# Kernel tuning notes

Measured on AMD Instinct MI355X. Metric: run time of the kernel, lower is better.

## Reference

```python
import jax, jax.numpy as jnp
import numpy as np

HID, NH, HD = 1024, 16, 64
WIN = 512
DFF, NE, TOPK = 4096, 8, 2
B, S = 1, 2048
EPS = 1e-6


def _rope_rotation_matrix(seq_len, head_dim):
    # Block-diagonal 2x2 rotation matrices per position (standard RoPE as a fused matrix).
    pos = np.arange(seq_len, dtype=np.float64)
    inv_freq = 1.0 / (10000.0 ** (np.arange(0, head_dim, 2, dtype=np.float64) / head_dim))
    ang = pos[:, None] * inv_freq[None, :]            # [S, HD/2]
    c, s = np.cos(ang), np.sin(ang)
    R = np.zeros((seq_len, head_dim, head_dim), np.float32)
    i = np.arange(0, head_dim, 2)
    R[:, i, i] = c
    R[:, i + 1, i + 1] = c
    R[:, i, i + 1] = -s
    R[:, i + 1, i] = s
    return jnp.asarray(R)


def setup_inputs() -> dict:
    key = jax.random.key(0)
    ks = jax.random.split(key, 10)
    init = lambda k, shape, scale=0.02: (jax.random.normal(k, shape, jnp.float32) * scale)
    return {
        "x": jax.random.normal(ks[0], (B, S, HID), jnp.float32),
        "rotation_matrix": _rope_rotation_matrix(S, HD),
        "rms1_w": jnp.ones((HID,), jnp.float32),
        "wq": init(ks[1], (HID, HID)),
        "wk": init(ks[2], (HID, HID)),
        "wv": init(ks[3], (HID, HID)),
        "wo": init(ks[4], (HID, HID)),
        "rms2_w": jnp.ones((HID,), jnp.float32),
        "gate_w": init(ks[5], (HID, NE)),
        "w1": init(ks[6], (NE, HID, DFF)),
        "w2": init(ks[7], (NE, DFF, HID)),
        "w3": init(ks[8], (NE, HID, DFF)),
    }


def _rmsnorm(x, w):
    return x * jax.lax.rsqrt(jnp.mean(x * x, axis=-1, keepdims=True) + EPS) * w


def reference(x, rotation_matrix, rms1_w, wq, wk, wv, wo, rms2_w, gate_w, w1, w2, w3):
    b, s, _ = x.shape
    # --- sliding-window attention with fused RoPE rotation matrix ---
    y = _rmsnorm(x, rms1_w)
    q = (y @ wq).reshape(b, s, NH, HD).transpose(0, 2, 1, 3)  # bhsd
    k = (y @ wk).reshape(b, s, NH, HD).transpose(0, 2, 1, 3)
    v = (y @ wv).reshape(b, s, NH, HD).transpose(0, 2, 1, 3)
    q = jnp.einsum('bhsd,sde->bhse', q, rotation_matrix)
    k = jnp.einsum('bhsd,sde->bhse', k, rotation_matrix)
    scores = jnp.einsum('bhqd,bhkd->bhqk', q, k) / np.float32(np.sqrt(HD))
    idx = jnp.arange(s)
    mask = (idx[:, None] >= idx[None, :]) & (idx[:, None] - idx[None, :] < WIN)
    scores = jnp.where(mask[None, None], scores, jnp.float32(-1e9))
    att = jax.nn.softmax(scores, axis=-1)
    attn_out = jnp.einsum('bhqk,bhkd->bhqd', att, v)
    attn_out = attn_out.transpose(0, 2, 1, 3).reshape(b, s, HID) @ wo
    x = x + attn_out
    # --- MoE SwiGLU FFN with top-k routing ---
    y = _rmsnorm(x, rms2_w)
    t = y.reshape(b * s, HID)                                  # [T, D]
    logits = t @ gate_w                                        # [T, E]
    top_v, top_i = jax.lax.top_k(logits, TOPK)
    gates = jax.nn.softmax(top_v, axis=-1)                     # [T, K]
    w_full = jnp.zeros((b * s, NE), t.dtype).at[
        jnp.arange(b * s)[:, None], top_i].set(gates)          # [T, E] sparse routing weights
    h = jax.nn.silu(jnp.einsum('td,edf->etf', t, w1)) * jnp.einsum('td,edf->etf', t, w3)
    expert_out = jnp.einsum('etf,efd->etd', h, w2)             # [E, T, D]
    moe = jnp.einsum('te,etd->td', w_full, expert_out).reshape(b, s, HID)
    return x + moe
```

## Files before the change

kernel.cpp:

```cpp
#include <hip/hip_runtime.h>
#include <hip/hip_bf16.h>
#include <stdint.h>


#define S_ 2048
#define HID_ 1024
#define NH_ 16
#define HD_ 64
#define WIN_ 512
#define DFF_ 4096
#define NE_ 8

typedef unsigned short u16;
typedef __attribute__((ext_vector_type(8))) short short8;
typedef __attribute__((ext_vector_type(4))) float f32x4;

__device__ __forceinline__ u16 f2bf(float f) {
  union { float f; unsigned u; } v; v.f = f;
  unsigned r = (v.u + 0x7FFFu + ((v.u >> 16) & 1u)) >> 16;
  return (u16)r;
}
__device__ __forceinline__ float bf2f(u16 b) {
  union { unsigned u; float f; } v; v.u = ((unsigned)b) << 16;
  return v.f;
}

__device__ __forceinline__ void gload16(const void* g, void* l) {
  __builtin_amdgcn_global_load_lds(
      (const __attribute__((address_space(1))) void*)g,
      (__attribute__((address_space(3))) void*)l, 16, 0, 0);
}

template <int N>
__device__ __forceinline__ void waitcnt_vm() {
  static_assert(N == 0 || N == 2 || N == 4 || N == 6 || N == 8 || N == 12 ||
                N == 16 || N == 24, "unsupported vmcnt");
  if constexpr (N == 0) asm volatile("s_waitcnt vmcnt(0)" ::: "memory");
  else if constexpr (N == 2) asm volatile("s_waitcnt vmcnt(2)" ::: "memory");
  else if constexpr (N == 4) asm volatile("s_waitcnt vmcnt(4)" ::: "memory");
  else if constexpr (N == 6) asm volatile("s_waitcnt vmcnt(6)" ::: "memory");
  else if constexpr (N == 8) asm volatile("s_waitcnt vmcnt(8)" ::: "memory");
  else if constexpr (N == 12) asm volatile("s_waitcnt vmcnt(12)" ::: "memory");
  else if constexpr (N == 16) asm volatile("s_waitcnt vmcnt(16)" ::: "memory");
  else if constexpr (N == 24) asm volatile("s_waitcnt vmcnt(24)" ::: "memory");
}

__global__ __launch_bounds__(512) void convT_f32_k(const float* __restrict__ Wa,
                                                   const float* __restrict__ Wb,
                                                   int zsplit,
                                                   u16* __restrict__ WT,
                                                   int K, int N, size_t matStride) {
  __shared__ alignas(16) char T[256 * 264];
  int z = blockIdx.z;
  const float* Wm = (z < zsplit ? Wa + (size_t)z * matStride
                                : Wb + (size_t)(z - zsplit) * matStride);
  u16* WTm = WT + (size_t)z * matStride;
  int n0 = blockIdx.x * 128, k0 = blockIdx.y * 256;
  int tid = threadIdx.x;
  int mq = tid & 31, tr_ = tid >> 5;
#pragma unroll
  for (int p = 0; p < 16; ++p) {
    int k = p * 16 + tr_;
    float4 v = *(const float4*)&Wm[(size_t)(k0 + k) * N + n0 + mq * 4];
    uint2 pk;
    pk.x = (unsigned)f2bf(v.x) | ((unsigned)f2bf(v.y) << 16);
    pk.y = (unsigned)f2bf(v.z) | ((unsigned)f2bf(v.w) << 16);
    *(uint2*)(T + k * 264 + ((mq ^ ((k >> 2) & 31)) << 3)) = pk;
  }
  __syncthreads();
#pragma unroll
  for (int p = 0; p < 8; ++p) {
    int n = p * 16 + tr_;
    int un = n >> 2, lo2 = (n & 3) * 2;
    short8 o;
#pragma unroll
    for (int j = 0; j < 8; ++j) {
      int k = mq * 8 + j;
      ((u16*)&o)[j] =
          *(const u16*)(T + k * 264 + ((un ^ ((k >> 2) & 31)) << 3) + lo2);
    }
    *(short8*)&WTm[(size_t)(n0 + n) * K + k0 + mq * 8] = o;
  }
}

__global__ __launch_bounds__(512) void convT_qkvo_k(const float* __restrict__ wq,
                                                    const float* __restrict__ wk,
                                                    const float* __restrict__ wv,
                                                    const float* __restrict__ wo,
                                                    u16* __restrict__ outT) {
  __shared__ alignas(16) char T[256 * 264];
  int z = blockIdx.z;
  const float* Wm = (z == 0) ? wq : (z == 1) ? wk : (z == 2) ? wv : wo;
  u16* WTm = outT + (size_t)z * HID_ * HID_;
  int n0 = blockIdx.x * 128, k0 = blockIdx.y * 256;
  int tid = threadIdx.x;
  int mq = tid & 31, tr_ = tid >> 5;
#pragma unroll
  for (int p = 0; p < 16; ++p) {
    int k = p * 16 + tr_;
    float4 v = *(const float4*)&Wm[(size_t)(k0 + k) * HID_ + n0 + mq * 4];
    uint2 pk;
    pk.x = (unsigned)f2bf(v.x) | ((unsigned)f2bf(v.y) << 16);
    pk.y = (unsigned)f2bf(v.z) | ((unsigned)f2bf(v.w) << 16);
    *(uint2*)(T + k * 264 + ((mq ^ ((k >> 2) & 31)) << 3)) = pk;
  }
  __syncthreads();
#pragma unroll
  for (int p = 0; p < 8; ++p) {
    int n = p * 16 + tr_;
    int un = n >> 2, lo2 = (n & 3) * 2;
    short8 o;
#pragma unroll
    for (int j = 0; j < 8; ++j) {
      int k = mq * 8 + j;
      ((u16*)&o)[j] =
          *(const u16*)(T + k * 264 + ((un ^ ((k >> 2) & 31)) << 3) + lo2);
    }
    *(short8*)&WTm[(size_t)(n0 + n) * HID_ + k0 + mq * 8] = o;
  }
}

__global__ __launch_bounds__(256) void convT_u16_k(const u16* __restrict__ W,
                                                   u16* __restrict__ WT,
                                                   int K, int N, size_t matStride) {
  __shared__ u16 t[64][66];
  const u16* Wm = W + (size_t)blockIdx.z * matStride;
  u16* WTm = WT + (size_t)blockIdx.z * matStride;
  int n0 = blockIdx.x * 64, k0 = blockIdx.y * 64;
  int tid = threadIdx.x;
  int c2 = (tid & 31) * 2, rr = tid >> 5;
#pragma unroll
  for (int it = 0; it < 8; ++it) {
    int r = it * 8 + rr;
    unsigned vv = *(const unsigned*)&Wm[(size_t)(k0 + r) * N + n0 + c2];
    t[c2][r] = (u16)vv;
    t[c2 + 1][r] = (u16)(vv >> 16);
  }
  __syncthreads();
#pragma unroll
  for (int it = 0; it < 8; ++it) {
    int n = it * 8 + rr;
    unsigned pk = (unsigned)t[n][c2] | ((unsigned)t[n][c2 + 1] << 16);
    *(unsigned*)&WTm[(size_t)(n0 + n) * K + k0 + c2] = pk;
  }
}

__global__ __launch_bounds__(256) void rms1_rope_k(const float* __restrict__ x,
                                                   const float* __restrict__ rw,
                                                   u16* __restrict__ y,
                                                   const float* __restrict__ rot,
                                                   float* __restrict__ cost,
                                                   float* __restrict__ sint) {
  int b = blockIdx.x, tid = threadIdx.x;
  if (b >= S_) {
    int id = (b - S_) * 256 + tid;
    if (id < S_ * 32) {
      int s = id >> 5, j = id & 31;
      cost[id] = rot[(size_t)s * 4096 + (size_t)(2 * j) * 64 + 2 * j];
      sint[id] = rot[(size_t)s * 4096 + (size_t)(2 * j + 1) * 64 + 2 * j];
    }
    return;
  }
  int row = b;
  const float4 v = *(const float4*)&x[(size_t)row * HID_ + tid * 4];
  float ss = v.x * v.x + v.y * v.y + v.z * v.z + v.w * v.w;
#pragma unroll
  for (int o = 32; o; o >>= 1) ss += __shfl_xor(ss, o);
  __shared__ float red[4];
  if ((tid & 63) == 0) red[tid >> 6] = ss;
  __syncthreads();
  float rstd = rsqrtf((red[0] + red[1] + red[2] + red[3]) * (1.f / HID_) + 1e-6f);
  const float4 w4 = *(const float4*)&rw[tid * 4];
  ushort4 o4;
  o4.x = f2bf(v.x * rstd * w4.x);
  o4.y = f2bf(v.y * rstd * w4.y);
  o4.z = f2bf(v.z * rstd * w4.z);
  o4.w = f2bf(v.w * rstd * w4.w);
  *(ushort4*)&y[(size_t)row * HID_ + tid * 4] = o4;
}

__global__ __launch_bounds__(256) void rms2_gate_k(const float* __restrict__ x2,
                                                   const float* __restrict__ rw,
                                                   const float* __restrict__ gw,
                                                   u16* __restrict__ y2,
                                                   float* __restrict__ logits) {
  int row = blockIdx.x, tid = threadIdx.x;
  int wv = tid >> 6, ln = tid & 63;
  const float4 v = *(const float4*)&x2[(size_t)row * HID_ + tid * 4];
  float ss = v.x * v.x + v.y * v.y + v.z * v.z + v.w * v.w;
#pragma unroll
  for (int o = 32; o; o >>= 1) ss += __shfl_xor(ss, o);
  __shared__ float red[4];
  __shared__ float lred[4][8];
  if (ln == 0) red[wv] = ss;
  __syncthreads();
  float rstd = rsqrtf((red[0] + red[1] + red[2] + red[3]) * (1.f / HID_) + 1e-6f);
  const float4 w4 = *(const float4*)&rw[tid * 4];
  float yv[4];
  yv[0] = v.x * rstd * w4.x; yv[1] = v.y * rstd * w4.y;
  yv[2] = v.z * rstd * w4.z; yv[3] = v.w * rstd * w4.w;
  ushort4 o4;
  o4.x = f2bf(yv[0]); o4.y = f2bf(yv[1]); o4.z = f2bf(yv[2]); o4.w = f2bf(yv[3]);
  *(ushort4*)&y2[(size_t)row * HID_ + tid * 4] = o4;
  float le[8] = {0, 0, 0, 0, 0, 0, 0, 0};
  int d0 = tid * 4;
#pragma unroll
  for (int j = 0; j < 4; ++j) {
    const float* grow = &gw[(size_t)(d0 + j) * NE_];
#pragma unroll
    for (int e = 0; e < 8; ++e) le[e] += yv[j] * grow[e];
  }
#pragma unroll
  for (int e = 0; e < 8; ++e) {
    float t = le[e];
#pragma unroll
    for (int o = 32; o; o >>= 1) t += __shfl_xor(t, o);
    le[e] = t;
  }
  if (ln == 0)
#pragma unroll
    for (int e = 0; e < 8; ++e) lred[wv][e] = le[e];
  __syncthreads();
  if (tid < 8)
    logits[(size_t)row * NE_ + tid] =
        lred[0][tid] + lred[1][tid] + lred[2][tid] + lred[3][tid];
}

__global__ __launch_bounds__(1024) void route_k(const float* __restrict__ logits,
                                                int* __restrict__ topi,
                                                float* __restrict__ topg,
                                                int* __restrict__ counts,
                                                int* __restrict__ ebase,
                                                int* __restrict__ slot_token,
                                                int* __restrict__ slot_of) {
  __shared__ int cnt[8], bas[8], rnk[8];
  int tid = threadIdx.x;
  if (tid < 8) { cnt[tid] = 0; rnk[tid] = 0; }
  __syncthreads();
  int e0[2], e1[2];
  float g0[2], g1[2];
#pragma unroll
  for (int s = 0; s < 2; ++s) {
    int t = tid * 2 + s;
    const float* lg = &logits[(size_t)t * NE_];
    float v0 = -1e30f; int i0 = 0;
#pragma unroll
    for (int e = 0; e < 8; ++e) {
      float x = lg[e];
      if (x > v0) { v0 = x; i0 = e; }
    }
    float v1 = -1e30f; int i1 = 0;
#pragma unroll
    for (int e = 0; e < 8; ++e) {
      if (e == i0) continue;
      float x = lg[e];
      if (x > v1) { v1 = x; i1 = e; }
    }
    float ex = __expf(v1 - v0);
    e0[s] = i0; e1[s] = i1;
    g0[s] = 1.f / (1.f + ex);
    g1[s] = ex / (1.f + ex);
    topi[t * 2] = i0; topi[t * 2 + 1] = i1;
    topg[t * 2] = g0[s]; topg[t * 2 + 1] = g1[s];
    atomicAdd(&cnt[i0], 1);
    atomicAdd(&cnt[i1], 1);
  }
  __syncthreads();
  if (tid == 0) {
    int s = 0;
    for (int e = 0; e < 8; ++e) { bas[e] = s; s += cnt[e]; }
  }
  __syncthreads();
#pragma unroll
  for (int s = 0; s < 2; ++s) {
    int t = tid * 2 + s;
    int p0 = bas[e0[s]] + atomicAdd(&rnk[e0[s]], 1);
    int p1 = bas[e1[s]] + atomicAdd(&rnk[e1[s]], 1);
    slot_token[p0] = t; slot_token[p1] = t;
    slot_of[t * 2] = p0; slot_of[t * 2 + 1] = p1;
  }
  if (tid < 8) { counts[tid] = cnt[tid]; ebase[tid] = bas[tid]; }
}

template <int MODE, int SLOTS>
__global__ __launch_bounds__(256, (SLOTS <= 3 ? 3 : (SLOTS <= 5 ? 2 : 1)))
void gemm3_k(
    const u16* __restrict__ A, const u16* __restrict__ B0,
    const u16* __restrict__ B1, const u16* __restrict__ B2, int K,
    const int* __restrict__ ecnt, const int* __restrict__ ebase,
    const float* __restrict__ cost, const float* __restrict__ sint,
    const float* __restrict__ xres, float* __restrict__ outf,
    u16* __restrict__ o0, u16* __restrict__ o1, u16* __restrict__ o2) {
  constexpr int WVM = 4 * (SLOTS - 2);
  __shared__ alignas(16) char smem[SLOTS * 16384];

  int n0 = blockIdx.x * 128, m0 = blockIdx.y * 128;
  int cnt = 0, base = 0, kc = 0;
  const u16* Bp;
  u16* outb = o0;
  float* pout = outf;
  int rope = 0;
  if constexpr (MODE == 0) {
    int z = blockIdx.z;
    Bp = (z == 0) ? B0 : (z == 1) ? B1 : B2;
    outb = (z == 0) ? o0 : (z == 1) ? o1 : o2;
    rope = (z < 2) ? 1 : 0;
  } else if constexpr (MODE == 1) {
    Bp = B0;
  } else if constexpr (MODE == 4) {
    int e = blockIdx.z >> 1;
    kc = blockIdx.z & 1;
    cnt = ecnt[e]; base = ebase[e];
    if (m0 >= cnt) return;
    Bp = B0 + (size_t)e * HID_ * DFF_;
    pout = outf + (size_t)kc * ((size_t)2 * S_ * HID_);
  } else {
    int e = blockIdx.z;
    cnt = ecnt[e]; base = ebase[e];
    if (m0 >= cnt) return;
    Bp = B0 + (size_t)e * HID_ * DFF_;
  }

  int tid = threadIdx.x, w = tid >> 6, l = tid & 63, lo = l & 15, g = l >> 4;
  int wm = w >> 1, wn = w & 1;
  int KT = K >> 5;
  size_t rb = (MODE == 4) ? (size_t)DFF_ * 2 : (size_t)K * 2;
  size_t kcoff = (MODE == 4) ? (size_t)kc * (size_t)(DFF_ / 2) * 2 : 0;

  int lrow = l >> 2, lu = l & 3;
  const char* pA[2];
  const char* pB[2];
  int ldOff[2];
#pragma unroll
  for (int j = 0; j < 2; ++j) {
    int rA = j * 64 + w * 16 + lrow;
    int swz = (lu ^ ((rA >> 1) & 3)) << 4;
    size_t arow;
    if constexpr (MODE == 3 || MODE == 4) {
      arow = (size_t)(base + min(m0 + rA, cnt - 1));
    } else {
      arow = (size_t)(m0 + rA);
    }
    pA[j] = (const char*)A + arow * rb + kcoff + swz;
    pB[j] = (const char*)Bp + (size_t)(n0 + rA) * rb + kcoff + swz;
    ldOff[j] = (j * 64 + w * 16) * 64;
  }

  auto stage = [&](int t) {
    char* s = smem + (t % SLOTS) * 16384;
    size_t kb = (size_t)t * 64;
    gload16(pA[0] + kb, s + ldOff[0]);
    gload16(pA[1] + kb, s + ldOff[1]);
    gload16(pB[0] + kb, s + 8192 + ldOff[0]);
    gload16(pB[1] + kb, s + 8192 + ldOff[1]);
  };

  f32x4 acc[4][4];
#pragma unroll
  for (int i = 0; i < 4; ++i)
#pragma unroll
    for (int j = 0; j < 4; ++j) acc[i][j] = (f32x4){0.f, 0.f, 0.f, 0.f};

#pragma unroll
  for (int s = 0; s < SLOTS - 1; ++s) stage(min(s, KT - 1));
  waitcnt_vm<WVM>();
  __builtin_amdgcn_s_barrier();

  for (int t = 0; t < KT; ++t) {
    char* s = smem + (t % SLOTS) * 16384;
    stage(min(t + SLOTS - 1, KT - 1));
    short8 afr[4], bfr[4];
#pragma unroll
    for (int mi = 0; mi < 4; ++mi) {
      int r = wm * 64 + mi * 16 + lo;
      afr[mi] = *(const short8*)(s + r * 64 + ((g ^ ((r >> 1) & 3)) << 4));
    }
#pragma unroll
    for (int ni = 0; ni < 4; ++ni) {
      int r = wn * 64 + ni * 16 + lo;
      bfr[ni] = *(const short8*)(s + 8192 + r * 64 + ((g ^ ((r >> 1) & 3)) << 4));
    }
    asm volatile("s_waitcnt lgkmcnt(0)" ::: "memory");
    __builtin_amdgcn_s_setprio(1);
#pragma unroll
    for (int mi = 0; mi < 4; ++mi)
#pragma unroll
      for (int ni = 0; ni < 4; ++ni)
        acc[mi][ni] = __builtin_amdgcn_mfma_f32_16x16x32_bf16(afr[mi], bfr[ni], acc[mi][ni], 0, 0, 0);
    __builtin_amdgcn_s_setprio(0);
    if (t + 1 < KT)
      waitcnt_vm<WVM>();
    else
      waitcnt_vm<0>();
    __builtin_amdgcn_s_barrier();
  }
  asm volatile("s_waitcnt vmcnt(0) lgkmcnt(0)" ::: "memory");

#pragma unroll
  for (int mi = 0; mi < 4; ++mi) {
    int lr = wm * 64 + mi * 16 + g * 4;
#pragma unroll
    for (int ni = 0; ni < 4; ++ni) {
      int c = n0 + wn * 64 + ni * 16 + lo;
#pragma unroll
      for (int r = 0; r < 4; ++r) {
        float v = acc[mi][ni][r];
        if constexpr (MODE == 0) {
          int row = m0 + lr + r;
          float p = __shfl_xor(v, 1);
          if (rope) {
            int dd = c & 63;
            float co = cost[(size_t)row * 32 + (dd >> 1)];
            float si = sint[(size_t)row * 32 + (dd >> 1)];
            v = (dd & 1) ? (co * v - si * p) : (co * v + si * p);
          }
          outb[((size_t)(c >> 6) * S_ + row) * HD_ + (c & 63)] = f2bf(v);
        } else if constexpr (MODE == 1) {
          int row = m0 + lr + r;
          outf[(size_t)row * HID_ + c] = v + xres[(size_t)row * HID_ + c];
        } else if constexpr (MODE == 4) {
          int m = m0 + lr + r;
          if (m < cnt) pout[(size_t)(base + m) * HID_ + c] = v;
        } else {
          int m = m0 + lr + r;
          if (m < cnt) outb[(size_t)(base + m) * HID_ + c] = f2bf(v);
        }
      }
    }
  }
}

__global__ __launch_bounds__(512, 2) void gemm5_k(
    const u16* __restrict__ A, const u16* __restrict__ B0,
    const u16* __restrict__ B1, int K, const int* __restrict__ ecnt,
    const int* __restrict__ ebase, const int* __restrict__ slot_token,
    u16* __restrict__ o0, u16* __restrict__ o1) {
  constexpr int BM = 256;
  constexpr int MROW = 128;
  constexpr int MI = 8;
  constexpr int MH = 4;
  constexpr int ABYTES = BM * 128;
  __shared__ alignas(16) char smem[ABYTES * 4];
  char* ldsA = smem;
  char* ldsB = smem + 2 * ABYTES;

  int n0 = blockIdx.x * BM, m0 = blockIdx.y * BM;
  int e = blockIdx.z >> 1, mat = blockIdx.z & 1;
  int cnt = ecnt[e], base = ebase[e];
  if (m0 >= cnt) return;
  const u16* Bp = (mat ? B1 : B0) + (size_t)e * DFF_ * HID_;
  u16* outb = mat ? o1 : o0;

  int tid = threadIdx.x, w = tid >> 6, l = tid & 63, lo = l & 15, g = l >> 4;
  int wm = w >> 2, wn = w & 3;
  int KT = K >> 6;
  size_t rb = (size_t)K * 2;

  int lrow = l >> 3, lu = l & 7;
  const char* pA[4];
  const char* pB[4];
  int ldOff[4];
#pragma unroll
  for (int j = 0; j < 4; ++j) {
    int rA = j * 64 + w * 8 + lrow;
    int swz = (lu ^ (rA & 7)) << 4;
    size_t arow = (size_t)slot_token[base + min(m0 + rA, cnt - 1)];
    pA[j] = (const char*)A + arow * rb + swz;
    pB[j] = (const char*)Bp + (size_t)(n0 + rA) * rb + swz;
    ldOff[j] = (j * 64 + w * 8) * 128;
  }

  auto stA = [&](int t, int j) {
    gload16(pA[j] + (size_t)t * 128, ldsA + (t & 1) * ABYTES + ldOff[j]);
  };
  auto stB = [&](int t, int j) {
    gload16(pB[j] + (size_t)t * 128, ldsB + (t & 1) * ABYTES + ldOff[j]);
  };
  auto rdA = [&](int d, int mi, int kh) {
    int row = wm * MROW + mi * 16 + lo;
    return *(const short8*)(ldsA + d * ABYTES + row * 128 +
                            (((kh * 4 + g) ^ (row & 7)) << 4));
  };
  auto rdB = [&](int d, int ni, int kh) {
    int row = wn * 64 + ni * 16 + lo;
    return *(const short8*)(ldsB + d * ABYTES + row * 128 +
                            (((kh * 4 + g) ^ (row & 7)) << 4));
  };

  f32x4 acc[MI][4];
#pragma unroll
  for (int i = 0; i < MI; ++i)
#pragma unroll
    for (int j = 0; j < 4; ++j) acc[i][j] = (f32x4){0.f, 0.f, 0.f, 0.f};

  stB(0, 0); stB(0, 1); stB(0, 2); stB(0, 3);
  stA(0, 0); stA(0, 2); stA(0, 1); stA(0, 3);
  waitcnt_vm<2>();
  __builtin_amdgcn_s_barrier();

  for (int t = 0; t < KT; ++t) {
    int d = t & 1;
    int tn = min(t + 1, KT - 1);
    short8 afr[MH][2], bfr[4][2];
    stB(tn, 0); stB(tn, 1); stB(tn, 2); stB(tn, 3);
#pragma unroll
    for (int i = 0; i < MH; ++i) {
      afr[i][0] = rdA(d, i, 0);
      afr[i][1] = rdA(d, i, 1);
    }
#pragma unroll
    for (int n = 0; n < 4; ++n) {
      bfr[n][0] = rdB(d, n, 0);
      bfr[n][1] = rdB(d, n, 1);
    }
    asm volatile("s_waitcnt lgkmcnt(0)" ::: "memory");
    __builtin_amdgcn_s_setprio(1);
#pragma unroll
    for (int kh = 0; kh < 2; ++kh)
#pragma unroll
      for (int i = 0; i < MH; ++i)
#pragma unroll
        for (int n = 0; n < 4; ++n)
          acc[i][n] = __builtin_amdgcn_mfma_f32_16x16x32_bf16(
              afr[i][kh], bfr[n][kh], acc[i][n], 0, 0, 0);
    __builtin_amdgcn_s_setprio(0);
    waitcnt_vm<4>();
    __builtin_amdgcn_s_barrier();
    stA(tn, 0); stA(tn, 2); stA(tn, 1); stA(tn, 3);
#pragma unroll
    for (int i = 0; i < MH; ++i) {
      afr[i][0] = rdA(d, MH + i, 0);
      afr[i][1] = rdA(d, MH + i, 1);
    }
    asm volatile("s_waitcnt lgkmcnt(0)" ::: "memory");
    __builtin_amdgcn_s_setprio(1);
#pragma unroll
    for (int kh = 0; kh < 2; ++kh)
#pragma unroll
      for (int i = 0; i < MH; ++i)
#pragma unroll
        for (int n = 0; n < 4; ++n)
          acc[MH + i][n] = __builtin_amdgcn_mfma_f32_16x16x32_bf16(
              afr[i][kh], bfr[n][kh], acc[MH + i][n], 0, 0, 0);
    __builtin_amdgcn_s_setprio(0);
    waitcnt_vm<2>();
    __builtin_amdgcn_s_barrier();
  }
  asm volatile("s_waitcnt vmcnt(0) lgkmcnt(0)" ::: "memory");

#pragma unroll
  for (int mi = 0; mi < MI; ++mi) {
    int lr = wm * MROW + mi * 16 + g * 4;
#pragma unroll
    for (int ni = 0; ni < 4; ++ni) {
      int c = n0 + wn * 64 + ni * 16 + lo;
#pragma unroll
      for (int r = 0; r < 4; ++r) {
        int m = m0 + lr + r;
        if (m < cnt) outb[(size_t)(base + m) * DFF_ + c] = f2bf(acc[mi][ni][r]);
      }
    }
  }
}

__global__ __launch_bounds__(256) void swiglu_k(u16* __restrict__ h1,
                                                const u16* __restrict__ h3) {
  size_t i = ((size_t)blockIdx.x * 256 + threadIdx.x) * 8;
  short8 a = *(const short8*)(h1 + i);
  short8 b = *(const short8*)(h3 + i);
  short8 o;
#pragma unroll
  for (int j = 0; j < 8; ++j) {
    float x = bf2f((u16)a[j]), y = bf2f((u16)b[j]);
    float s = x / (1.f + __expf(-x));
    o[j] = (short)f2bf(s * y);
  }
  *(short8*)(h1 + i) = o;
}

__global__ __launch_bounds__(256) void attn_k(const u16* __restrict__ qh,
                                              const u16* __restrict__ kh,
                                              const u16* __restrict__ vht,
                                              u16* __restrict__ attn) {
  int qt = blockIdx.x, h = blockIdx.y;
  int tid = threadIdx.x, w = tid >> 6, l = tid & 63, lo = l & 15, g = l >> 4;
  __shared__ alignas(16) char Ks[8192];
  __shared__ alignas(16) char Vs[8192];
  __shared__ alignas(16) char Ps[8192];
  char* Pw = Ps + w * 2048;
  int q0 = qt * 64, qw = q0 + w * 16;
  const u16* qhh = qh + ((size_t)h * S_ + qw) * HD_;
  short8 bq0 = *(const short8*)(qhh + lo * 64 + g * 8);
  short8 bq1 = *(const short8*)(qhh + lo * 64 + 32 + g * 8);
  int q = qw + lo;
  float m_run = -1e30f, l_run = 0.f;
  f32x4 o[4];
#pragma unroll
  for (int i = 0; i < 4; ++i) o[i] = (f32x4){0.f, 0.f, 0.f, 0.f};
  int kt0 = max(0, q0 - (WIN_ - 1)) >> 6;
  for (int kt = kt0; kt <= qt; ++kt) {
    int kb = kt * 64;
    {
      int r0 = w * 16 + (l >> 3), r1 = r0 + 8;
      int uu = l & 7;
      short8 k0v = *(const short8*)(kh + ((size_t)h * S_ + kb + r0) * HD_ + uu * 8);
      short8 k1v = *(const short8*)(kh + ((size_t)h * S_ + kb + r1) * HD_ + uu * 8);
      short8 v0v = *(const short8*)(vht + ((size_t)h * HD_ + r0) * S_ + kb + uu * 8);
      short8 v1v = *(const short8*)(vht + ((size_t)h * HD_ + r1) * S_ + kb + uu * 8);
      *(short8*)(Ks + r0 * 128 + ((uu ^ (r0 & 7)) << 4)) = k0v;
      *(short8*)(Ks + r1 * 128 + ((uu ^ (r1 & 7)) << 4)) = k1v;
      *(short8*)(Vs + r0 * 128 + ((uu ^ (r0 & 7)) << 4)) = v0v;
      *(short8*)(Vs + r1 * 128 + ((uu ^ (r1 & 7)) << 4)) = v1v;
    }
    __syncthreads();
    f32x4 st[4];
#pragma unroll
    for (int kf = 0; kf < 4; ++kf) {
      int key = kf * 16 + lo;
      short8 a0 = *(const short8*)(Ks + key * 128 + ((g ^ (key & 7)) << 4));
      short8 a1 = *(const short8*)(Ks + key * 128 + (((4 + g) ^ (key & 7)) << 4));
      f32x4 z = (f32x4){0.f, 0.f, 0.f, 0.f};
      z = __builtin_amdgcn_mfma_f32_16x16x32_bf16(a0, bq0, z, 0, 0, 0);
      z = __builtin_amdgcn_mfma_f32_16x16x32_bf16(a1, bq1, z, 0, 0, 0);
      st[kf] = z;
    }
    float p[16];
    float tmax = -1e30f;
#pragma unroll
    for (int kf = 0; kf < 4; ++kf)
#pragma unroll
      for (int r = 0; r < 4; ++r) {
        int key = kb + kf * 16 + g * 4 + r;
        float s = st[kf][r] * 0.125f;
        bool okm = (key <= q) && (q - key < WIN_);
        s = okm ? s : -1e30f;
        p[kf * 4 + r] = s;
        tmax = fmaxf(tmax, s);
      }
    tmax = fmaxf(tmax, __shfl_xor(tmax, 16));
    tmax = fmaxf(tmax, __shfl_xor(tmax, 32));
    float m_new = fmaxf(m_run, tmax);
    float corr = __expf(m_run - m_new);
    float tsum = 0.f;
#pragma unroll
    for (int i = 0; i < 16; ++i) {
      float pe = (p[i] > -1e29f) ? __expf(p[i] - m_new) : 0.f;
      p[i] = pe;
      tsum += pe;
    }
    tsum += __shfl_xor(tsum, 16);
    tsum += __shfl_xor(tsum, 32);
    l_run = l_run * corr + tsum;
    m_run = m_new;
#pragma unroll
    for (int kf = 0; kf < 4; ++kf)
#pragma unroll
      for (int pr = 0; pr < 2; ++pr) {
        int keyloc = kf * 16 + g * 4 + pr * 2;
        unsigned pk = (unsigned)f2bf(p[kf * 4 + pr * 2]) |
                      ((unsigned)f2bf(p[kf * 4 + pr * 2 + 1]) << 16);
        *(unsigned*)(Pw + lo * 128 + (((keyloc >> 3) ^ (lo & 7)) << 4) +
                     (keyloc & 7) * 2) = pk;
      }
    float c0 = __shfl(corr, g * 4 + 0), c1 = __shfl(corr, g * 4 + 1);
    float c2 = __shfl(corr, g * 4 + 2), c3 = __shfl(corr, g * 4 + 3);
#pragma unroll
    for (int nf = 0; nf < 4; ++nf) {
      o[nf][0] *= c0; o[nf][1] *= c1; o[nf][2] *= c2; o[nf][3] *= c3;
    }
    short8 ap0 = *(const short8*)(Pw + lo * 128 + ((g ^ (lo & 7)) << 4));
    short8 ap1 = *(const short8*)(Pw + lo * 128 + (((4 + g) ^ (lo & 7)) << 4));
#pragma unroll
    for (int nf = 0; nf < 4; ++nf) {
      int d = nf * 16 + lo;
      short8 v0 = *(const short8*)(Vs + d * 128 + ((g ^ (d & 7)) << 4));
      short8 v1 = *(const short8*)(Vs + d * 128 + (((4 + g) ^ (d & 7)) << 4));
      o[nf] = __builtin_amdgcn_mfma_f32_16x16x32_bf16(ap0, v0, o[nf], 0, 0, 0);
      o[nf] = __builtin_amdgcn_mfma_f32_16x16x32_bf16(ap1, v1, o[nf], 0, 0, 0);
    }
    __syncthreads();
  }
  float linv = 1.f / l_run;
  float i0 = __shfl(linv, g * 4 + 0), i1 = __shfl(linv, g * 4 + 1);
  float i2 = __shfl(linv, g * 4 + 2), i3 = __shfl(linv, g * 4 + 3);
#pragma unroll
  for (int nf = 0; nf < 4; ++nf) {
    int d = nf * 16 + lo;
    attn[(size_t)(qw + g * 4 + 0) * HID_ + h * HD_ + d] = f2bf(o[nf][0] * i0);
    attn[(size_t)(qw + g * 4 + 1) * HID_ + h * HD_ + d] = f2bf(o[nf][1] * i1);
    attn[(size_t)(qw + g * 4 + 2) * HID_ + h * HD_ + d] = f2bf(o[nf][2] * i2);
    attn[(size_t)(qw + g * 4 + 3) * HID_ + h * HD_ + d] = f2bf(o[nf][3] * i3);
  }
}

__global__ __launch_bounds__(256) void combine_k(float* __restrict__ out,
                                                 const float* __restrict__ part,
                                                 const int* __restrict__ slot_of,
                                                 const float* __restrict__ topg) {
  int row = blockIdx.x, tid = threadIdx.x;
  int d0 = tid * 4;
  const size_t PS = (size_t)2 * S_ * HID_;
  int p0 = slot_of[row * 2], p1 = slot_of[row * 2 + 1];
  float g0 = topg[row * 2], g1 = topg[row * 2 + 1];
  float4 cur = *(float4*)&out[(size_t)row * HID_ + d0];
  float4 a0 = *(const float4*)&part[(size_t)p0 * HID_ + d0];
  float4 a1 = *(const float4*)&part[PS + (size_t)p0 * HID_ + d0];
  float4 b0 = *(const float4*)&part[(size_t)p1 * HID_ + d0];
  float4 b1 = *(const float4*)&part[PS + (size_t)p1 * HID_ + d0];
  cur.x += g0 * (a0.x + a1.x) + g1 * (b0.x + b1.x);
  cur.y += g0 * (a0.y + a1.y) + g1 * (b0.y + b1.y);
  cur.z += g0 * (a0.z + a1.z) + g1 * (b0.z + b1.z);
  cur.w += g0 * (a0.w + a1.w) + g1 * (b0.w + b1.w);
  *(float4*)&out[(size_t)row * HID_ + d0] = cur;
}

extern "C" void kernel_launch(void* const* d_in, const int* in_sizes, int n_in,
                              void* d_out, int out_size, void* d_ws,
                              size_t ws_size, hipStream_t stream) {
  const float* x = (const float*)d_in[0];
  const float* rot = (const float*)d_in[1];
  const float* r1w = (const float*)d_in[2];
  const float* wq = (const float*)d_in[3];
  const float* wk = (const float*)d_in[4];
  const float* wv = (const float*)d_in[5];
  const float* wo = (const float*)d_in[6];
  const float* r2w = (const float*)d_in[7];
  const float* gw = (const float*)d_in[8];
  const float* w1 = (const float*)d_in[9];
  const float* w2 = (const float*)d_in[10];
  const float* w3 = (const float*)d_in[11];
  float* out = (float*)d_out;

  char* ws = (char*)d_ws;
  size_t off = 0;
  auto alloc = [&](size_t bytes) {
    char* p = ws + off;
    off += (bytes + 255) & ~(size_t)255;
    return p;
  };
  const size_t MB4 = (size_t)S_ * HID_ * 2;
  u16* wqkvoT = (u16*)alloc((size_t)4 * HID_ * HID_ * 2);
  u16* wqT = wqkvoT;
  u16* wkT = wqkvoT + (size_t)HID_ * HID_;
  u16* wvT = wqkvoT + (size_t)2 * HID_ * HID_;
  u16* woT = wqkvoT + (size_t)3 * HID_ * HID_;
  u16* w13T = (u16*)alloc((size_t)2 * NE_ * DFF_ * HID_ * 2);
  u16* w1T = w13T;
  u16* w3T = w13T + (size_t)NE_ * DFF_ * HID_;
  u16* w2T = (u16*)alloc((size_t)NE_ * HID_ * DFF_ * 2);
  char* uni = alloc((size_t)2 * S_ * DFF_ * 2);
  u16* ybf = (u16*)(uni);
  u16* qh = (u16*)(uni + MB4);
  u16* kh = (u16*)(uni + 2 * MB4);
  u16* vh = (u16*)(uni + 3 * MB4);
  u16* vht = (u16*)(uni + 4 * MB4);
  u16* attnb = (u16*)(uni + 5 * MB4);
  u16* h3 = (u16*)uni;
  float* partials = (float*)uni;
  u16* y2bf = (u16*)alloc(MB4);
  u16* h1 = (u16*)alloc((size_t)2 * S_ * DFF_ * 2);
  float* cost = (float*)alloc((size_t)S_ * 32 * 4);
  float* sint = (float*)alloc((size_t)S_ * 32 * 4);
  float* logits = (float*)alloc((size_t)S_ * NE_ * 4);
  int* topi = (int*)alloc((size_t)S_ * 2 * 4);
  float* topg = (float*)alloc((size_t)S_ * 2 * 4);
  int* ints = (int*)alloc(256);
  int* counts = ints;
  int* ebase = ints + 8;
  int* slot_token = (int*)alloc((size_t)2 * S_ * 4);
  int* slot_of = (int*)alloc((size_t)S_ * 2 * 4);
  (void)ws_size; (void)in_sizes; (void)n_in; (void)out_size;

  convT_qkvo_k<<<dim3(8, 4, 4), 512, 0, stream>>>(wq, wk, wv, wo, wqkvoT);
  convT_f32_k<<<dim3(32, 4, 16), 512, 0, stream>>>(w1, w3, 8, w13T, HID_, DFF_,
                                                   (size_t)HID_ * DFF_);
  convT_f32_k<<<dim3(8, 16, 8), 512, 0, stream>>>(w2, nullptr, 8, w2T, DFF_,
                                                  HID_, (size_t)DFF_ * HID_);

  rms1_rope_k<<<dim3(S_ + 256), 256, 0, stream>>>(x, r1w, ybf, rot, cost, sint);

  gemm3_k<0, 5><<<dim3(8, 16, 3), 256, 0, stream>>>(
      ybf, wqT, wkT, wvT, HID_, nullptr, nullptr, cost, sint, nullptr,
      nullptr, qh, kh, vh);
  convT_u16_k<<<dim3(1, 32, 16), 256, 0, stream>>>(vh, vht, S_, HD_, (size_t)S_ * HD_);

  attn_k<<<dim3(32, 16), 256, 0, stream>>>(qh, kh, vht, attnb);

  gemm3_k<1, 5><<<dim3(8, 16, 1), 256, 0, stream>>>(
      attnb, woT, nullptr, nullptr, HID_, nullptr, nullptr, nullptr, nullptr,
      x, out, nullptr, nullptr, nullptr);

  rms2_gate_k<<<dim3(S_), 256, 0, stream>>>(out, r2w, gw, y2bf, logits);
  route_k<<<dim3(1), 1024, 0, stream>>>(logits, topi, topg, counts, ebase,
                                        slot_token, slot_of);

  gemm5_k<<<dim3(16, 4, 16), 512, 0, stream>>>(
      y2bf, w1T, w3T, HID_, counts, ebase, slot_token, h1, h3);
  swiglu_k<<<dim3(8192), 256, 0, stream>>>(h1, h3);
  gemm3_k<4, 4><<<dim3(8, 16, 16), 256, 0, stream>>>(
      h1, w2T, nullptr, nullptr, DFF_ / 2, counts, ebase, nullptr, nullptr,
      nullptr, partials, nullptr, nullptr, nullptr);
  combine_k<<<dim3(S_), 256, 0, stream>>>(out, partials, slot_of, topg);
}
```

Measured before the change: 423.2 us.

## Restructure expert up-projection GEMM into finer-grained quadrant pipeline with staggered loads

Rewrites the main loop of the MoE w1/w3 GEMM kernel to handle two K-tiles per iteration. Each tile is split into four MFMA quadrants with LDS reads and half-tile global-to-LDS loads interleaved between barriers, and B loads are issued one tile further ahead. Launch bounds drop to one block per SIMD group, so more registers are available for the fragment buffers. The aim is better overlap of memory traffic with matrix math. The cost is more barriers per tile and lower occupancy.

```diff
diff --git a/kernel.cpp b/kernel.cpp
--- a/kernel.cpp
+++ b/kernel.cpp
@@ -430,15 +430,14 @@
   }
 }
 
-__global__ __launch_bounds__(512, 2) void gemm5_k(
-    const u16* __restrict__ A, const u16* __restrict__ B0,
-    const u16* __restrict__ B1, int K, const int* __restrict__ ecnt,
+__global__ __launch_bounds__(512, 1) void gemm5_k(
+    const u16* __restrict__ A, const u16* __restrict__ B0m,
+    const u16* __restrict__ B1m, int K, const int* __restrict__ ecnt,
     const int* __restrict__ ebase, const int* __restrict__ slot_token,
     u16* __restrict__ o0, u16* __restrict__ o1) {
   constexpr int BM = 256;
   constexpr int MROW = 128;
   constexpr int MI = 8;
-  constexpr int MH = 4;
   constexpr int ABYTES = BM * 128;
   __shared__ alignas(16) char smem[ABYTES * 4];
   char* ldsA = smem;
@@ -448,7 +447,7 @@
   int e = blockIdx.z >> 1, mat = blockIdx.z & 1;
   int cnt = ecnt[e], base = ebase[e];
   if (m0 >= cnt) return;
-  const u16* Bp = (mat ? B1 : B0) + (size_t)e * DFF_ * HID_;
+  const u16* Bp = (mat ? B1m : B0m) + (size_t)e * DFF_ * HID_;
   u16* outb = mat ? o1 : o0;
 
   int tid = threadIdx.x, w = tid >> 6, l = tid & 63, lo = l & 15, g = l >> 4;
@@ -470,11 +469,15 @@
     ldOff[j] = (j * 64 + w * 8) * 128;
   }
 
-  auto stA = [&](int t, int j) {
-    gload16(pA[j] + (size_t)t * 128, ldsA + (t & 1) * ABYTES + ldOff[j]);
+  auto stA2 = [&](int uc, int s, int h) {
+    char* dst = ldsA + s * ABYTES;
+    gload16(pA[2 * h] + (size_t)uc * 128, dst + ldOff[2 * h]);
+    gload16(pA[2 * h + 1] + (size_t)uc * 128, dst + ldOff[2 * h + 1]);
   };
-  auto stB = [&](int t, int j) {
-    gload16(pB[j] + (size_t)t * 128, ldsB + (t & 1) * ABYTES + ldOff[j]);
+  auto stB2 = [&](int uc, int s, int h) {
+    char* dst = ldsB + s * ABYTES;
+    gload16(pB[2 * h] + (size_t)uc * 128, dst + ldOff[2 * h]);
+    gload16(pB[2 * h + 1] + (size_t)uc * 128, dst + ldOff[2 * h + 1]);
   };
   auto rdA = [&](int d, int mi, int kh) {
     int row = wm * MROW + mi * 16 + lo;
@@ -493,57 +496,168 @@
 #pragma unroll
     for (int j = 0; j < 4; ++j) acc[i][j] = (f32x4){0.f, 0.f, 0.f, 0.f};
 
-  stB(0, 0); stB(0, 1); stB(0, 2); stB(0, 3);
-  stA(0, 0); stA(0, 2); stA(0, 1); stA(0, 3);
-  waitcnt_vm<2>();
+  stB2(0, 0, 0); stB2(0, 0, 1);
+  stA2(0, 0, 0); stA2(0, 0, 1);
+  stB2(1, 1, 0); stB2(1, 1, 1);
+  waitcnt_vm<4>();
   __builtin_amdgcn_s_barrier();
 
-  for (int t = 0; t < KT; ++t) {
-    int d = t & 1;
-    int tn = min(t + 1, KT - 1);
-    short8 afr[MH][2], bfr[4][2];
-    stB(tn, 0); stB(tn, 1); stB(tn, 2); stB(tn, 3);
-#pragma unroll
-    for (int i = 0; i < MH; ++i) {
-      afr[i][0] = rdA(d, i, 0);
-      afr[i][1] = rdA(d, i, 1);
-    }
-#pragma unroll
-    for (int n = 0; n < 4; ++n) {
-      bfr[n][0] = rdB(d, n, 0);
-      bfr[n][1] = rdB(d, n, 1);
-    }
+  short8 afr[4][2], bA[2][2], bB[2][2];
+
+  for (int t = 0; t < KT; t += 2) {
+    int u2 = min(t + 2, KT - 1);
+    int u3 = min(t + 3, KT - 1);
+#pragma unroll
+    for (int i = 0; i < 4; ++i) {
+      afr[i][0] = rdA(0, i, 0);
+      afr[i][1] = rdA(0, i, 1);
+    }
+#pragma unroll
+    for (int n = 0; n < 2; ++n) {
+      bA[n][0] = rdB(0, n, 0);
+      bA[n][1] = rdB(0, n, 1);
+    }
+    stA2(t + 1, 1, 0);
+    __builtin_amdgcn_s_barrier();
     asm volatile("s_waitcnt lgkmcnt(0)" ::: "memory");
     __builtin_amdgcn_s_setprio(1);
 #pragma unroll
     for (int kh = 0; kh < 2; ++kh)
 #pragma unroll
-      for (int i = 0; i < MH; ++i)
-#pragma unroll
-        for (int n = 0; n < 4; ++n)
+      for (int i = 0; i < 4; ++i)
+#pragma unroll
+        for (int n = 0; n < 2; ++n)
           acc[i][n] = __builtin_amdgcn_mfma_f32_16x16x32_bf16(
-              afr[i][kh], bfr[n][kh], acc[i][n], 0, 0, 0);
+              afr[i][kh], bA[n][kh], acc[i][n], 0, 0, 0);
+    __builtin_amdgcn_s_setprio(0);
+    __builtin_amdgcn_s_barrier();
+#pragma unroll
+    for (int n = 0; n < 2; ++n) {
+      bB[n][0] = rdB(0, n + 2, 0);
+      bB[n][1] = rdB(0, n + 2, 1);
+    }
+    stA2(t + 1, 1, 1);
+    __builtin_amdgcn_s_barrier();
+    asm volatile("s_waitcnt lgkmcnt(0)" ::: "memory");
+    __builtin_amdgcn_s_setprio(1);
+#pragma unroll
+    for (int kh = 0; kh < 2; ++kh)
+#pragma unroll
+      for (int i = 0; i < 4; ++i)
+#pragma unroll
+        for (int n = 0; n < 2; ++n)
+          acc[i][n + 2] = __builtin_amdgcn_mfma_f32_16x16x32_bf16(
+              afr[i][kh], bB[n][kh], acc[i][n + 2], 0, 0, 0);
+    __builtin_amdgcn_s_setprio(0);
+    __builtin_amdgcn_s_barrier();
+#pragma unroll
+    for (int i = 0; i < 4; ++i) {
+      afr[i][0] = rdA(0, i + 4, 0);
+      afr[i][1] = rdA(0, i + 4, 1);
+    }
+    stB2(u2, 0, 0);
+    __builtin_amdgcn_s_barrier();
+    asm volatile("s_waitcnt lgkmcnt(0)" ::: "memory");
+    __builtin_amdgcn_s_setprio(1);
+#pragma unroll
+    for (int kh = 0; kh < 2; ++kh)
+#pragma unroll
+      for (int i = 0; i < 4; ++i)
+#pragma unroll
+        for (int n = 0; n < 2; ++n)
+          acc[i + 4][n + 2] = __builtin_amdgcn_mfma_f32_16x16x32_bf16(
+              afr[i][kh], bB[n][kh], acc[i + 4][n + 2], 0, 0, 0);
+    __builtin_amdgcn_s_setprio(0);
+    __builtin_amdgcn_s_barrier();
+    stB2(u2, 0, 1);
+    __builtin_amdgcn_s_barrier();
+    __builtin_amdgcn_s_setprio(1);
+#pragma unroll
+    for (int kh = 0; kh < 2; ++kh)
+#pragma unroll
+      for (int i = 0; i < 4; ++i)
+#pragma unroll
+        for (int n = 0; n < 2; ++n)
+          acc[i + 4][n] = __builtin_amdgcn_mfma_f32_16x16x32_bf16(
+              afr[i][kh], bA[n][kh], acc[i + 4][n], 0, 0, 0);
     __builtin_amdgcn_s_setprio(0);
     waitcnt_vm<4>();
     __builtin_amdgcn_s_barrier();
-    stA(tn, 0); stA(tn, 2); stA(tn, 1); stA(tn, 3);
-#pragma unroll
-    for (int i = 0; i < MH; ++i) {
-      afr[i][0] = rdA(d, MH + i, 0);
-      afr[i][1] = rdA(d, MH + i, 1);
-    }
+#pragma unroll
+    for (int i = 0; i < 4; ++i) {
+      afr[i][0] = rdA(1, i, 0);
+      afr[i][1] = rdA(1, i, 1);
+    }
+#pragma unroll
+    for (int n = 0; n < 2; ++n) {
+      bA[n][0] = rdB(1, n, 0);
+      bA[n][1] = rdB(1, n, 1);
+    }
+    stA2(u2, 0, 0);
+    __builtin_amdgcn_s_barrier();
     asm volatile("s_waitcnt lgkmcnt(0)" ::: "memory");
     __builtin_amdgcn_s_setprio(1);
 #pragma unroll
     for (int kh = 0; kh < 2; ++kh)
 #pragma unroll
-      for (int i = 0; i < MH; ++i)
-#pragma unroll
-        for (int n = 0; n < 4; ++n)
-          acc[MH + i][n] = __builtin_amdgcn_mfma_f32_16x16x32_bf16(
-              afr[i][kh], bfr[n][kh], acc[MH + i][n], 0, 0, 0);
+      for (int i = 0; i < 4; ++i)
+#pragma unroll
+        for (int n = 0; n < 2; ++n)
+          acc[i][n] = __builtin_amdgcn_mfma_f32_16x16x32_bf16(
+              afr[i][kh], bA[n][kh], acc[i][n], 0, 0, 0);
     __builtin_amdgcn_s_setprio(0);
-    waitcnt_vm<2>();
+    __builtin_amdgcn_s_barrier();
+#pragma unroll
+    for (int n = 0; n < 2; ++n) {
+      bB[n][0] = rdB(1, n + 2, 0);
+      bB[n][1] = rdB(1, n + 2, 1);
+    }
+    stA2(u2, 0, 1);
+    __builtin_amdgcn_s_barrier();
+    asm volatile("s_waitcnt lgkmcnt(0)" ::: "memory");
+    __builtin_amdgcn_s_setprio(1);
+#pragma unroll
+    for (int kh = 0; kh < 2; ++kh)
+#pragma unroll
+      for (int i = 0; i < 4; ++i)
+#pragma unroll
+        for (int n = 0; n < 2; ++n)
+          acc[i][n + 2] = __builtin_amdgcn_mfma_f32_16x16x32_bf16(
+              afr[i][kh], bB[n][kh], acc[i][n + 2], 0, 0, 0);
+    __builtin_amdgcn_s_setprio(0);
+    __builtin_amdgcn_s_barrier();
+#pragma unroll
+    for (int i = 0; i < 4; ++i) {
+      afr[i][0] = rdA(1, i + 4, 0);
+      afr[i][1] = rdA(1, i + 4, 1);
+    }
+    stB2(u3, 1, 0);
+    __builtin_amdgcn_s_barrier();
+    asm volatile("s_waitcnt lgkmcnt(0)" ::: "memory");
+    __builtin_amdgcn_s_setprio(1);
+#pragma unroll
+    for (int kh = 0; kh < 2; ++kh)
+#pragma unroll
+      for (int i = 0; i < 4; ++i)
+#pragma unroll
+        for (int n = 0; n < 2; ++n)
+          acc[i + 4][n + 2] = __builtin_amdgcn_mfma_f32_16x16x32_bf16(
+              afr[i][kh], bB[n][kh], acc[i + 4][n + 2], 0, 0, 0);
+    __builtin_amdgcn_s_setprio(0);
+    __builtin_amdgcn_s_barrier();
+    stB2(u3, 1, 1);
+    __builtin_amdgcn_s_barrier();
+    __builtin_amdgcn_s_setprio(1);
+#pragma unroll
+    for (int kh = 0; kh < 2; ++kh)
+#pragma unroll
+      for (int i = 0; i < 4; ++i)
+#pragma unroll
+        for (int n = 0; n < 2; ++n)
+          acc[i + 4][n] = __builtin_amdgcn_mfma_f32_16x16x32_bf16(
+              afr[i][kh], bA[n][kh], acc[i + 4][n], 0, 0, 0);
+    __builtin_amdgcn_s_setprio(0);
+    waitcnt_vm<4>();
     __builtin_amdgcn_s_barrier();
   }
   asm volatile("s_waitcnt vmcnt(0) lgkmcnt(0)" ::: "memory");
```

Result: no change. 421.3 us (-0.5%).
